# Optimization experiments

Hardware: AMD Instinct MI355X
Metric: run time of the kernel (lower is better)

Reference implementation:

```python
import jax, jax.numpy as jnp
import numpy as np

N_NODES = 20000
N_EDGES = 640000
D_NODE = 128
D_EDGE = 64
D_OUT = 128


def setup_inputs() -> dict:
    key = jax.random.key(0)
    ks = jax.random.split(key, 7)
    feats_node = jax.random.normal(ks[0], (N_NODES, D_NODE), dtype=jnp.float32)
    feats_edge = jax.random.normal(ks[1], (N_EDGES, D_EDGE), dtype=jnp.float32)
    # nn.init.normal_(std=0.5) on all three linear weights
    Wn = 0.5 * jax.random.normal(ks[2], (D_OUT, D_NODE), dtype=jnp.float32)
    We = 0.5 * jax.random.normal(ks[3], (D_OUT, D_EDGE), dtype=jnp.float32)
    Wa = 0.5 * jax.random.normal(ks[4], (1, 3 * D_OUT), dtype=jnp.float32)
    src = jax.random.randint(ks[5], (N_EDGES,), 0, N_NODES, dtype=jnp.int32)
    dst = jax.random.randint(ks[6], (N_EDGES,), 0, N_NODES, dtype=jnp.int32)
    return {"feats_node": feats_node, "feats_edge": feats_edge,
            "Wn": Wn, "We": We, "Wa": Wa, "src": src, "dst": dst}


def reference(feats_node, feats_edge, Wn, We, Wa, src, dst):
    n_nodes = feats_node.shape[0]
    d = Wn.shape[0]
    # dense projections: z_node [N, d], z_edge [E, d]
    z_node = feats_node @ Wn.T
    z_edge = feats_edge @ We.T
    # split attn weight so we never materialize the [E, 3d] concat
    a_src, a_dst, a_e = Wa[0, :d], Wa[0, d:2 * d], Wa[0, 2 * d:]
    z_src = z_node[src]                       # [E, d] gather
    z_dst = z_node[dst]                       # [E, d] gather
    logits = z_src @ a_src + z_dst @ a_dst + z_edge @ a_e   # [E]
    e = jax.nn.leaky_relu(logits, negative_slope=0.2)
    # segment softmax over incoming edges of each dst node
    m = jax.ops.segment_max(e, dst, num_segments=n_nodes)   # [N]
    ex = jnp.exp(e - m[dst])                                 # [E]
    s = jax.ops.segment_sum(ex, dst, num_segments=n_nodes)  # [N]
    alpha = ex / jnp.where(s[dst] == 0, 1.0, s[dst])         # [E]
    # weighted scatter-sum of src features into dst nodes
    h = jax.ops.segment_sum(alpha[:, None] * z_src, dst, num_segments=n_nodes)
    return h
```

## Files before the change

### kernel.cpp

```cpp
#include <hip/hip_runtime.h>
#include <hip/hip_bf16.h>

#define N_NODES 20000
#define N_EDGES 640000
#define D_NODE  128
#define D_EDGE  64
#define D_OUT   128

__device__ __forceinline__ unsigned short f2bf(float x) {
    unsigned u = __float_as_uint(x);
    unsigned r = ((u >> 16) & 1u) + 0x7FFFu;
    return (unsigned short)((u + r) >> 16);
}
__device__ __forceinline__ float bf2f(unsigned short b) {
    return __uint_as_float((unsigned)b << 16);
}

__global__ __launch_bounds__(256) void k_init_prep(const float* __restrict__ Wn,
                                                   const float* __restrict__ We,
                                                   const float* __restrict__ Wa,
                                                   int* __restrict__ deg,
                                                   float* __restrict__ WnT,
                                                   float* __restrict__ ce) {
    int t = threadIdx.x, b = blockIdx.x;
    if (b < 79) {
        int i = b * 256 + t;
        if (i < N_NODES) deg[i] = 0;
    } else {
        for (int idx = t; idx < D_OUT * D_NODE; idx += 256) {
            int o = idx >> 7, k = idx & 127;
            WnT[k * D_OUT + o] = Wn[idx];
        }
        if (t < D_EDGE) {
            float a = 0.f;
            for (int o = 0; o < D_OUT; ++o)
                a += Wa[2 * D_OUT + o] * We[o * D_EDGE + t];
            ce[t] = a;
        }
    }
}

__global__ __launch_bounds__(256) void k_fused(const float* __restrict__ feats,
                                               const float* __restrict__ wT,
                                               const float* __restrict__ Wa,
                                               const float* __restrict__ fe,
                                               const float* __restrict__ ce,
                                               const int* __restrict__ dst,
                                               unsigned short* __restrict__ zb,
                                               float* __restrict__ ssrc,
                                               float* __restrict__ sdst,
                                               int* __restrict__ deg,
                                               int* __restrict__ rank,
                                               float* __restrict__ ge) {
    __shared__ float sW[32 * 128];
    __shared__ float sF[32 * 128];
    int t = threadIdx.x;

    if (blockIdx.x >= 625) {
        int b = blockIdx.x - 625;
        int j = b * 64 + (t >> 2);
        int part = t & 3;
        const float4* row = (const float4*)(fe + (size_t)j * D_EDGE + part * 16);
        const float4* c4 = (const float4*)(ce + part * 16);
        float acc = 0.f;
#pragma unroll
        for (int i = 0; i < 4; ++i) {
            float4 f = row[i];
            float4 c = c4[i];
            acc += f.x * c.x + f.y * c.y + f.z * c.z + f.w * c.w;
        }
        acc += __shfl_xor(acc, 1, 64);
        acc += __shfl_xor(acc, 2, 64);
        if (part == 0) {
            ge[j] = acc;
            rank[j] = atomicAdd(&deg[dst[j]], 1);
        }
        return;
    }

    int nb = blockIdx.x * 32;
    const float4* fsrc = (const float4*)(feats + (size_t)nb * D_NODE);
    float4* fdst = (float4*)sF;
    for (int i = t; i < 32 * 32; i += 256) fdst[i] = fsrc[i];

    float acc[4][4] = {{0.f}};
    int o0 = (t & 31) * 4;
    int n0 = (t >> 5) * 4;

    for (int p = 0; p < 4; ++p) {
        __syncthreads();
        const float4* wsrc = (const float4*)(wT + p * 32 * 128);
        float4* wdst = (float4*)sW;
        for (int i = t; i < 32 * 32; i += 256) wdst[i] = wsrc[i];
        __syncthreads();
        for (int kk = 0; kk < 32; kk += 4) {
            float4 w0 = *(const float4*)(sW + (kk + 0) * 128 + o0);
            float4 w1 = *(const float4*)(sW + (kk + 1) * 128 + o0);
            float4 w2 = *(const float4*)(sW + (kk + 2) * 128 + o0);
            float4 w3 = *(const float4*)(sW + (kk + 3) * 128 + o0);
#pragma unroll
            for (int j = 0; j < 4; ++j) {
                float4 f = *(const float4*)(sF + (n0 + j) * 128 + p * 32 + kk);
                acc[j][0] += f.x * w0.x + f.y * w1.x + f.z * w2.x + f.w * w3.x;
                acc[j][1] += f.x * w0.y + f.y * w1.y + f.z * w2.y + f.w * w3.y;
                acc[j][2] += f.x * w0.z + f.y * w1.z + f.z * w2.z + f.w * w3.z;
                acc[j][3] += f.x * w0.w + f.y * w1.w + f.z * w2.w + f.w * w3.w;
            }
        }
    }

    float as0 = Wa[o0 + 0], as1 = Wa[o0 + 1], as2 = Wa[o0 + 2], as3 = Wa[o0 + 3];
    float ad0 = Wa[128 + o0 + 0], ad1 = Wa[128 + o0 + 1],
          ad2 = Wa[128 + o0 + 2], ad3 = Wa[128 + o0 + 3];
#pragma unroll
    for (int j = 0; j < 4; ++j) {
        int n = nb + n0 + j;
        ushort4 zo;
        zo.x = f2bf(acc[j][0]); zo.y = f2bf(acc[j][1]);
        zo.z = f2bf(acc[j][2]); zo.w = f2bf(acc[j][3]);
        *(ushort4*)(zb + (size_t)n * D_OUT + o0) = zo;
        float ps = acc[j][0] * as0 + acc[j][1] * as1 + acc[j][2] * as2 + acc[j][3] * as3;
        float pd = acc[j][0] * ad0 + acc[j][1] * ad1 + acc[j][2] * ad2 + acc[j][3] * ad3;
#pragma unroll
        for (int off = 16; off; off >>= 1) {
            ps += __shfl_xor(ps, off, 32);
            pd += __shfl_xor(pd, off, 32);
        }
        if ((t & 31) == 0) { ssrc[n] = ps; sdst[n] = pd; }
    }
}

__global__ __launch_bounds__(1024) void k_scan(const int* __restrict__ deg,
                                               int* __restrict__ offsets) {
    __shared__ int wsum[16];
    __shared__ int woff[16];
    const int PER = 20;
    int t = threadIdx.x, lane = t & 63, wv = t >> 6;
    int base = t * PER;
    int v[PER];
    int tsum = 0;
#pragma unroll
    for (int i = 0; i < PER; ++i) {
        int idx = base + i;
        v[i] = (idx < N_NODES) ? deg[idx] : 0;
        tsum += v[i];
    }
    int x = tsum;
#pragma unroll
    for (int d = 1; d < 64; d <<= 1) {
        int y = __shfl_up(x, d, 64);
        if (lane >= d) x += y;
    }
    if (lane == 63) wsum[wv] = x;
    __syncthreads();
    if (t == 0) {
        int a = 0;
        for (int i = 0; i < 16; ++i) { int tmp = wsum[i]; woff[i] = a; a += tmp; }
        offsets[N_NODES] = a;
    }
    __syncthreads();
    int run = (x - tsum) + woff[wv];
#pragma unroll
    for (int i = 0; i < PER; ++i) {
        int idx = base + i;
        if (idx < N_NODES) offsets[idx] = run;
        run += v[i];
    }
}

__global__ __launch_bounds__(256) void k_place(const float* __restrict__ ge,
                                               const float* __restrict__ ssrc,
                                               const float* __restrict__ sdst,
                                               const int* __restrict__ src,
                                               const int* __restrict__ dst,
                                               const int* __restrict__ rank,
                                               const int* __restrict__ offsets,
                                               float2* __restrict__ es) {
    int j = blockIdx.x * 256 + threadIdx.x;
    int sj = src[j], dj = dst[j];
    float x = ge[j] + ssrc[sj] + sdst[dj];
    float ev = x > 0.f ? x : 0.2f * x;
    int pos = offsets[dj] + rank[j];
    es[pos] = make_float2(ev, __int_as_float(sj));
}

__global__ __launch_bounds__(256) void k_gather(const int* __restrict__ offsets,
                                                const float2* __restrict__ es,
                                                const unsigned short* __restrict__ zb,
                                                float* __restrict__ h) {
    int lane = threadIdx.x & 63;
    int n = blockIdx.x * 4 + (threadIdx.x >> 6);
    int beg = offsets[n], end = offsets[n + 1];

    float2 v0 = make_float2(-3.4e38f, 0.f);
    int i0 = beg + lane;
    if (i0 < end) v0 = es[i0];
    float lmax = v0.x;
    for (int base = beg + 64; base < end; base += 64) {
        int i = base + lane;
        lmax = fmaxf(lmax, (i < end) ? es[i].x : -3.4e38f);
    }
#pragma unroll
    for (int off = 32; off; off >>= 1) lmax = fmaxf(lmax, __shfl_xor(lmax, off, 64));
    float m = lmax;

    float w0 = (i0 < end) ? __expf(v0.x - m) : 0.f;
    float lsum = w0;
    for (int base = beg + 64; base < end; base += 64) {
        int i = base + lane;
        lsum += (i < end) ? __expf(es[i].x - m) : 0.f;
    }
#pragma unroll
    for (int off = 32; off; off >>= 1) lsum += __shfl_xor(lsum, off, 64);
    float inv = (lsum > 0.f) ? 1.f / lsum : 0.f;

    float accx = 0.f, accy = 0.f;
    {
        int cnt = min(64, end - beg);
        float wl = w0 * inv;
        int sl = __float_as_int(v0.y);
        int r = 0;
        for (; r + 4 <= cnt; r += 4) {
            float wr0 = __shfl(wl, r + 0, 64); int sr0 = __shfl(sl, r + 0, 64);
            float wr1 = __shfl(wl, r + 1, 64); int sr1 = __shfl(sl, r + 1, 64);
            float wr2 = __shfl(wl, r + 2, 64); int sr2 = __shfl(sl, r + 2, 64);
            float wr3 = __shfl(wl, r + 3, 64); int sr3 = __shfl(sl, r + 3, 64);
            ushort2 z0 = *(const ushort2*)(zb + (size_t)sr0 * D_OUT + lane * 2);
            ushort2 z1 = *(const ushort2*)(zb + (size_t)sr1 * D_OUT + lane * 2);
            ushort2 z2 = *(const ushort2*)(zb + (size_t)sr2 * D_OUT + lane * 2);
            ushort2 z3 = *(const ushort2*)(zb + (size_t)sr3 * D_OUT + lane * 2);
            accx += wr0 * bf2f(z0.x) + wr1 * bf2f(z1.x) + wr2 * bf2f(z2.x) + wr3 * bf2f(z3.x);
            accy += wr0 * bf2f(z0.y) + wr1 * bf2f(z1.y) + wr2 * bf2f(z2.y) + wr3 * bf2f(z3.y);
        }
        for (; r < cnt; ++r) {
            float wr = __shfl(wl, r, 64); int sr = __shfl(sl, r, 64);
            ushort2 zv = *(const ushort2*)(zb + (size_t)sr * D_OUT + lane * 2);
            accx += wr * bf2f(zv.x); accy += wr * bf2f(zv.y);
        }
    }
    for (int base = beg + 64; base < end; base += 64) {
        int i = base + lane;
        float2 v = (i < end) ? es[i] : make_float2(0.f, 0.f);
        float wl = (i < end) ? __expf(v.x - m) * inv : 0.f;
        int sl = __float_as_int(v.y);
        int cnt = min(64, end - base);
        int r = 0;
        for (; r + 4 <= cnt; r += 4) {
            float wr0 = __shfl(wl, r + 0, 64); int sr0 = __shfl(sl, r + 0, 64);
            float wr1 = __shfl(wl, r + 1, 64); int sr1 = __shfl(sl, r + 1, 64);
            float wr2 = __shfl(wl, r + 2, 64); int sr2 = __shfl(sl, r + 2, 64);
            float wr3 = __shfl(wl, r + 3, 64); int sr3 = __shfl(sl, r + 3, 64);
            ushort2 z0 = *(const ushort2*)(zb + (size_t)sr0 * D_OUT + lane * 2);
            ushort2 z1 = *(const ushort2*)(zb + (size_t)sr1 * D_OUT + lane * 2);
            ushort2 z2 = *(const ushort2*)(zb + (size_t)sr2 * D_OUT + lane * 2);
            ushort2 z3 = *(const ushort2*)(zb + (size_t)sr3 * D_OUT + lane * 2);
            accx += wr0 * bf2f(z0.x) + wr1 * bf2f(z1.x) + wr2 * bf2f(z2.x) + wr3 * bf2f(z3.x);
            accy += wr0 * bf2f(z0.y) + wr1 * bf2f(z1.y) + wr2 * bf2f(z2.y) + wr3 * bf2f(z3.y);
        }
        for (; r < cnt; ++r) {
            float wr = __shfl(wl, r, 64); int sr = __shfl(sl, r, 64);
            ushort2 zv = *(const ushort2*)(zb + (size_t)sr * D_OUT + lane * 2);
            accx += wr * bf2f(zv.x); accy += wr * bf2f(zv.y);
        }
    }
    *(float2*)(h + (size_t)n * D_OUT + lane * 2) = make_float2(accx, accy);
}

extern "C" void kernel_launch(void* const* d_in, const int* in_sizes, int n_in,
                              void* d_out, int out_size, void* d_ws, size_t ws_size,
                              hipStream_t stream) {
    const float* feats_node = (const float*)d_in[0];
    const float* feats_edge = (const float*)d_in[1];
    const float* Wn = (const float*)d_in[2];
    const float* We = (const float*)d_in[3];
    const float* Wa = (const float*)d_in[4];
    const int* src = (const int*)d_in[5];
    const int* dst = (const int*)d_in[6];
    float* h = (float*)d_out;

    float* WnT  = (float*)d_ws;
    float* ce   = WnT + 16384;
    float* ssrc = ce + 64;
    float* sdst = ssrc + N_NODES;
    float2* es  = (float2*)(sdst + N_NODES);
    unsigned short* zb = (unsigned short*)(es + N_EDGES);
    int* deg     = (int*)(zb + (size_t)N_NODES * D_OUT);
    int* offsets = deg + N_NODES;
    int* rank    = offsets + N_NODES + 1;
    float* ge    = (float*)(rank + N_EDGES);

    k_init_prep<<<80, 256, 0, stream>>>(Wn, We, Wa, deg, WnT, ce);
    k_fused<<<625 + N_EDGES / 64, 256, 0, stream>>>(feats_node, WnT, Wa, feats_edge, ce,
                                                    dst, zb, ssrc, sdst, deg, rank, ge);
    k_scan<<<1, 1024, 0, stream>>>(deg, offsets);
    k_place<<<N_EDGES / 256, 256, 0, stream>>>(ge, ssrc, sdst, src, dst, rank, offsets, es);
    k_gather<<<N_NODES / 4, 256, 0, stream>>>(offsets, es, zb, h);
}
```

Measured before the change: 336.2 us.

## Fold degree scan into last edge block of fused kernel via completion counter

Removes the separate single-block scan kernel launch. The last of the edge blocks to finish (detected with a global atomic counter and threadfence) computes the exclusive prefix sum of degrees in place. The init kernel is also parallelised so the weight transpose is spread across blocks and the edge-attention reduction is split over 256 threads. The scan now runs on a 256-thread block rather than 1024 threads, and it adds an atomic per edge block.

Result: slower. 747.9 us (+122.4%).

```diff
diff --git a/kernel.cpp b/kernel.cpp
--- a/kernel.cpp
+++ b/kernel.cpp
@@ -21,22 +21,28 @@
                                                    const float* __restrict__ Wa,
                                                    int* __restrict__ deg,
                                                    float* __restrict__ WnT,
-                                                   float* __restrict__ ce) {
+                                                   float* __restrict__ ce,
+                                                   int* __restrict__ done) {
     int t = threadIdx.x, b = blockIdx.x;
-    if (b < 79) {
-        int i = b * 256 + t;
-        if (i < N_NODES) deg[i] = 0;
-    } else {
-        for (int idx = t; idx < D_OUT * D_NODE; idx += 256) {
-            int o = idx >> 7, k = idx & 127;
-            WnT[k * D_OUT + o] = Wn[idx];
-        }
-        if (t < D_EDGE) {
-            float a = 0.f;
-            for (int o = 0; o < D_OUT; ++o)
-                a += Wa[2 * D_OUT + o] * We[o * D_EDGE + t];
-            ce[t] = a;
-        }
+    int gid = b * 256 + t;
+    if (gid < N_NODES) deg[gid] = 0;
+    if (gid == 0) *done = 0;
+    if (gid < D_OUT * D_NODE) {
+        int o = gid >> 7, k = gid & 127;
+        WnT[k * D_OUT + o] = Wn[gid];
+    }
+    if (b == 79) {
+        __shared__ float tmp[256];
+        int e = t & 63, p = t >> 6;
+        float a = 0.f;
+#pragma unroll
+        for (int oo = 0; oo < 32; ++oo) {
+            int o = p * 32 + oo;
+            a += Wa[2 * D_OUT + o] * We[o * D_EDGE + e];
+        }
+        tmp[t] = a;
+        __syncthreads();
+        if (t < 64) ce[t] = tmp[t] + tmp[t + 64] + tmp[t + 128] + tmp[t + 192];
     }
 }
 
@@ -51,7 +57,9 @@
                                                float* __restrict__ sdst,
                                                int* __restrict__ deg,
                                                int* __restrict__ rank,
-                                               float* __restrict__ ge) {
+                                               float* __restrict__ ge,
+                                               int* __restrict__ done,
+                                               int* __restrict__ offsets) {
     __shared__ float sW[32 * 128];
     __shared__ float sF[32 * 128];
     int t = threadIdx.x;
@@ -74,6 +82,52 @@
         if (part == 0) {
             ge[j] = acc;
             rank[j] = atomicAdd(&deg[dst[j]], 1);
+        }
+
+        __shared__ int lastflag;
+        __syncthreads();
+        if (t == 0) {
+            __threadfence();
+            lastflag = (atomicAdd(done, 1) == 10000 - 1) ? 1 : 0;
+        }
+        __syncthreads();
+        if (!lastflag) return;
+
+        __shared__ int wsum[4];
+        __shared__ int woff[4];
+        const int PER = 80;
+        int lane = t & 63, wv = t >> 6;
+        int base = t * PER;
+        int sum = 0;
+        for (int i = 0; i < PER; ++i) {
+            int idx = base + i;
+            if (idx < N_NODES)
+                sum += __hip_atomic_load(&deg[idx], __ATOMIC_RELAXED,
+                                         __HIP_MEMORY_SCOPE_AGENT);
+        }
+        int x = sum;
+#pragma unroll
+        for (int d = 1; d < 64; d <<= 1) {
+            int y = __shfl_up(x, d, 64);
+            if (lane >= d) x += y;
+        }
+        if (lane == 63) wsum[wv] = x;
+        __syncthreads();
+        if (t == 0) {
+            int a = 0;
+            for (int i = 0; i < 4; ++i) { int w = wsum[i]; woff[i] = a; a += w; }
+            offsets[N_NODES] = a;
+        }
+        __syncthreads();
+        int run = (x - sum) + woff[wv];
+        for (int i = 0; i < PER; ++i) {
+            int idx = base + i;
+            if (idx < N_NODES) {
+                int dv = __hip_atomic_load(&deg[idx], __ATOMIC_RELAXED,
+                                           __HIP_MEMORY_SCOPE_AGENT);
+                offsets[idx] = run;
+                run += dv;
+            }
         }
         return;
     }
@@ -127,44 +181,6 @@
             pd += __shfl_xor(pd, off, 32);
         }
         if ((t & 31) == 0) { ssrc[n] = ps; sdst[n] = pd; }
-    }
-}
-
-__global__ __launch_bounds__(1024) void k_scan(const int* __restrict__ deg,
-                                               int* __restrict__ offsets) {
-    __shared__ int wsum[16];
-    __shared__ int woff[16];
-    const int PER = 20;
-    int t = threadIdx.x, lane = t & 63, wv = t >> 6;
-    int base = t * PER;
-    int v[PER];
-    int tsum = 0;
-#pragma unroll
-    for (int i = 0; i < PER; ++i) {
-        int idx = base + i;
-        v[i] = (idx < N_NODES) ? deg[idx] : 0;
-        tsum += v[i];
-    }
-    int x = tsum;
-#pragma unroll
-    for (int d = 1; d < 64; d <<= 1) {
-        int y = __shfl_up(x, d, 64);
-        if (lane >= d) x += y;
-    }
-    if (lane == 63) wsum[wv] = x;
-    __syncthreads();
-    if (t == 0) {
-        int a = 0;
-        for (int i = 0; i < 16; ++i) { int tmp = wsum[i]; woff[i] = a; a += tmp; }
-        offsets[N_NODES] = a;
-    }
-    __syncthreads();
-    int run = (x - tsum) + woff[wv];
-#pragma unroll
-    for (int i = 0; i < PER; ++i) {
-        int idx = base + i;
-        if (idx < N_NODES) offsets[idx] = run;
-        run += v[i];
     }
 }
 
@@ -288,11 +304,12 @@
     int* offsets = deg + N_NODES;
     int* rank    = offsets + N_NODES + 1;
     float* ge    = (float*)(rank + N_EDGES);
-
-    k_init_prep<<<80, 256, 0, stream>>>(Wn, We, Wa, deg, WnT, ce);
+    int* done    = (int*)(ge + N_EDGES);
+
+    k_init_prep<<<80, 256, 0, stream>>>(Wn, We, Wa, deg, WnT, ce, done);
     k_fused<<<625 + N_EDGES / 64, 256, 0, stream>>>(feats_node, WnT, Wa, feats_edge, ce,
-                                                    dst, zb, ssrc, sdst, deg, rank, ge);
-    k_scan<<<1, 1024, 0, stream>>>(deg, offsets);
+                                                    dst, zb, ssrc, sdst, deg, rank, ge,
+                                                    done, offsets);
     k_place<<<N_EDGES / 256, 256, 0, stream>>>(ge, ssrc, sdst, src, dst, rank, offsets, es);
     k_gather<<<N_NODES / 4, 256, 0, stream>>>(offsets, es, zb, h);
 }
```
